# Performance work log

Measured on AMD Instinct MI355X. Metric: run time of the kernel, lower is better.

## Reference

```python
import jax, jax.numpy as jnp
import numpy as np

N = 100000      # nodes
E = 1600000     # edges (avg degree 16)
D = 128         # feature dim (in_dim == out_dim)
ALPHA = 0.1     # initial-residual mixing
BETA = 0.5      # identity-mapping / linear mixing


def setup_inputs() -> dict:
    key = jax.random.key(0)
    k1, k2, k3, k4, k5 = jax.random.split(key, 5)
    features = jax.random.normal(k1, (N, D), dtype=jnp.float32)
    initial_features = jax.random.normal(k2, (N, D), dtype=jnp.float32)
    # xavier_uniform with relu gain sqrt(2): bound = gain * sqrt(6/(fan_in+fan_out))
    bound = np.sqrt(2.0) * np.sqrt(6.0 / (D + D))
    W = jax.random.uniform(k5, (D, D), dtype=jnp.float32, minval=-bound, maxval=bound)
    src = jax.random.randint(k3, (E,), 0, N, dtype=jnp.int32)
    dst = jax.random.randint(k4, (E,), 0, N, dtype=jnp.int32)
    return {"features": features, "initial_features": initial_features,
            "W": W, "src": src, "dst": dst}


def reference(features, initial_features, W, src, dst):
    # symmetric degree normalization (edge weights are all ones)
    degs = jax.ops.segment_sum(jnp.ones((E,), features.dtype), dst, num_segments=N)
    norm = jnp.power(jnp.maximum(degs, 1.0), -0.5)[:, None]          # [N,1]
    h = features * norm                                               # [N,D]
    # message passing: m_e = h[src_e] * w_e (w=1); aggregate sum into dst
    agg = jax.ops.segment_sum(h[src], dst, num_segments=N)            # [N,D]
    h = agg * norm
    # alpha initial-residual, beta identity-mapped linear combine
    h = (1.0 - ALPHA) * h + ALPHA * initial_features
    h = (1.0 - BETA) * h + BETA * (h @ W.T)
    return jax.nn.relu(h)
```

## Files before the change

### kernel.cpp

```cpp
#include <hip/hip_runtime.h>
#include <math.h>

#define D 128
#define THREADS 256
#define BS 512
#define MAXB 1024
#define BIN_T 512
#define BIN_CHUNK 4096

typedef __attribute__((ext_vector_type(8))) short s16x8;
typedef __attribute__((ext_vector_type(4))) float f32x4;

__device__ __forceinline__ unsigned short f2bf(float f) {
    unsigned u = __float_as_uint(f);
    u += 0x7FFFu + ((u >> 16) & 1u);
    return (unsigned short)(u >> 16);
}
__device__ __forceinline__ float bflo(unsigned u) { return __uint_as_float(u << 16); }
__device__ __forceinline__ float bfhi(unsigned u) { return __uint_as_float(u & 0xFFFF0000u); }


__global__ __launch_bounds__(THREADS) void k_hist(const int* __restrict__ dst,
                                                  int* __restrict__ bcnt,
                                                  int E, int nbuck) {
    __shared__ int lh[MAXB];
    for (int b = threadIdx.x; b < nbuck; b += THREADS) lh[b] = 0;
    __syncthreads();
    const int stride = gridDim.x * THREADS;
    for (int e = blockIdx.x * THREADS + threadIdx.x; e < E; e += stride)
        atomicAdd(&lh[dst[e] >> 9], 1);
    __syncthreads();
    for (int b = threadIdx.x; b < nbuck; b += THREADS) {
        const int v = lh[b];
        if (v) atomicAdd(&bcnt[b], v);
    }
}

__global__ __launch_bounds__(MAXB) void k_scan(const int* __restrict__ bcnt,
                                               int* __restrict__ bbase,
                                               int* __restrict__ bcur, int nbuck) {
    __shared__ int sh[MAXB];
    const int tid = threadIdx.x;
    const int v = (tid < nbuck) ? bcnt[tid] : 0;
    sh[tid] = v;
    __syncthreads();
    for (int s = 1; s < MAXB; s <<= 1) {
        const int t = (tid >= s) ? sh[tid - s] : 0;
        __syncthreads();
        sh[tid] += t;
        __syncthreads();
    }
    if (tid < nbuck) {
        const int ex = sh[tid] - v;
        bbase[tid] = ex;
        bcur[tid] = ex;
    }
    if (tid == nbuck - 1) bbase[nbuck] = sh[tid];
}

__global__ __launch_bounds__(BIN_T) void k_bin(const int* __restrict__ src,
                                               const int* __restrict__ dst,
                                               int* __restrict__ bcur,
                                               int2* __restrict__ ebuf,
                                               int E, int nbuck) {
    __shared__ int lh[MAXB];
    __shared__ int lbase[MAXB];
    const int tid = threadIdx.x;
    for (int b = tid; b < nbuck; b += BIN_T) lh[b] = 0;
    __syncthreads();
    const int base = blockIdx.x * BIN_CHUNK;
    int2 ed[8];
#pragma unroll
    for (int k = 0; k < 8; ++k) {
        const int e = base + k * BIN_T + tid;
        if (e < E) {
            ed[k] = make_int2(dst[e], src[e]);
            atomicAdd(&lh[ed[k].x >> 9], 1);
        } else {
            ed[k].x = -1;
        }
    }
    __syncthreads();
    for (int b = tid; b < nbuck; b += BIN_T) {
        const int v = lh[b];
        lbase[b] = v ? atomicAdd(&bcur[b], v) : 0;
        lh[b] = 0;
    }
    __syncthreads();
#pragma unroll
    for (int k = 0; k < 8; ++k) {
        if (ed[k].x >= 0) {
            const int b = ed[k].x >> 9;
            const int pos = lbase[b] + atomicAdd(&lh[b], 1);
            ebuf[pos] = ed[k];
        }
    }
}

__global__ __launch_bounds__(BS) void k_csr(const int* __restrict__ bbase,
                                            const int2* __restrict__ ebuf,
                                            int* __restrict__ csr,
                                            int* __restrict__ off,
                                            float* __restrict__ normf,
                                            int n, int nbuck) {
    __shared__ int cnt[BS];
    __shared__ int ex[BS];
    const int b = blockIdx.x, tid = threadIdx.x;
    const int lo = bbase[b], hi = bbase[b + 1];
    cnt[tid] = 0;
    __syncthreads();
    for (int e = lo + tid; e < hi; e += BS)
        atomicAdd(&cnt[ebuf[e].x & (BS - 1)], 1);
    __syncthreads();
    const int deg = cnt[tid];
    ex[tid] = deg;
    __syncthreads();
    for (int s = 1; s < BS; s <<= 1) {
        const int t = (tid >= s) ? ex[tid - s] : 0;
        __syncthreads();
        ex[tid] += t;
        __syncthreads();
    }
    const int excl = ex[tid] - deg;
    const int node = b * BS + tid;
    if (node < n) {
        off[node] = lo + excl;
        normf[node] = rsqrtf(fmaxf((float)deg, 1.0f));
    }
    if (b == nbuck - 1 && tid == 0) off[n] = bbase[nbuck];
    cnt[tid] = excl;
    __syncthreads();
    for (int e = lo + tid; e < hi; e += BS) {
        const int2 edge = ebuf[e];
        const int p = atomicAdd(&cnt[edge.x & (BS - 1)], 1);
        csr[lo + p] = edge.y;
    }
}

__global__ __launch_bounds__(THREADS) void k_scale(
    const float* __restrict__ f, const float* __restrict__ nrm,
    uint4* __restrict__ hb, int n) {
    int c = blockIdx.x * THREADS + threadIdx.x;
    if (c >= n * 16) return;
    float nv = nrm[c >> 4];
    const float4* fp = (const float4*)f;
    float4 a = fp[c * 2], b = fp[c * 2 + 1];
    uint4 o;
    o.x = f2bf(a.x * nv) | ((unsigned)f2bf(a.y * nv) << 16);
    o.y = f2bf(a.z * nv) | ((unsigned)f2bf(a.w * nv) << 16);
    o.z = f2bf(b.x * nv) | ((unsigned)f2bf(b.y * nv) << 16);
    o.w = f2bf(b.z * nv) | ((unsigned)f2bf(b.w * nv) << 16);
    hb[c] = o;
}

__global__ __launch_bounds__(THREADS) void k_gather_csr(
    const uint4* __restrict__ hb, const float* __restrict__ initf,
    const int* __restrict__ off, const int* __restrict__ csr,
    const float* __restrict__ normf, uint4* __restrict__ tb, int n) {
    const int g = (blockIdx.x * THREADS + threadIdx.x) >> 4;
    if (g >= n) return;
    const int gl = threadIdx.x & 15;

    float acc[8] = {0.f, 0.f, 0.f, 0.f, 0.f, 0.f, 0.f, 0.f};

#define ROW(S)                                                      \
    {                                                               \
        const uint4 r = hb[(size_t)(S)*16 + gl];                    \
        acc[0] += bflo(r.x); acc[1] += bfhi(r.x);                   \
        acc[2] += bflo(r.y); acc[3] += bfhi(r.y);                   \
        acc[4] += bflo(r.z); acc[5] += bfhi(r.z);                   \
        acc[6] += bflo(r.w); acc[7] += bfhi(r.w);                   \
    }
    const int begin = off[g], end = off[g + 1];
    int j = begin;
    for (; j + 4 <= end; j += 4) {
        const int s0 = csr[j], s1 = csr[j + 1], s2 = csr[j + 2], s3 = csr[j + 3];
        ROW(s0); ROW(s1); ROW(s2); ROW(s3);
    }
    for (; j < end; ++j) ROW(csr[j]);
#undef ROW

    const float nv = 0.9f * normf[g];
    const float4* iv = (const float4*)(initf + (size_t)g * D);
    const float4 i0 = iv[gl * 2], i1 = iv[gl * 2 + 1];
    float t[8];
    t[0] = nv * acc[0] + 0.1f * i0.x; t[1] = nv * acc[1] + 0.1f * i0.y;
    t[2] = nv * acc[2] + 0.1f * i0.z; t[3] = nv * acc[3] + 0.1f * i0.w;
    t[4] = nv * acc[4] + 0.1f * i1.x; t[5] = nv * acc[5] + 0.1f * i1.y;
    t[6] = nv * acc[6] + 0.1f * i1.z; t[7] = nv * acc[7] + 0.1f * i1.w;
    uint4 o;
    o.x = f2bf(t[0]) | ((unsigned)f2bf(t[1]) << 16);
    o.y = f2bf(t[2]) | ((unsigned)f2bf(t[3]) << 16);
    o.z = f2bf(t[4]) | ((unsigned)f2bf(t[5]) << 16);
    o.w = f2bf(t[6]) | ((unsigned)f2bf(t[7]) << 16);
    tb[(size_t)g * 16 + gl] = o;
}

__device__ __forceinline__ void stage_M(const float* __restrict__ W,
                                        uint4* __restrict__ sMt, int tid) {
    for (int c = tid; c < D * 16; c += THREADS) {
        const int j = c >> 4, kc = c & 15;
        const float* wr = W + j * D + kc * 8;
        float m[8];
#pragma unroll
        for (int q = 0; q < 8; ++q) m[q] = 0.5f * wr[q];
        const int dj = j - kc * 8;
        if (dj >= 0 && dj < 8) m[dj] += 0.5f;
        uint4 o;
        o.x = f2bf(m[0]) | ((unsigned)f2bf(m[1]) << 16);
        o.y = f2bf(m[2]) | ((unsigned)f2bf(m[3]) << 16);
        o.z = f2bf(m[4]) | ((unsigned)f2bf(m[5]) << 16);
        o.w = f2bf(m[6]) | ((unsigned)f2bf(m[7]) << 16);
        sMt[j * 16 + (kc ^ (j & 7))] = o;
    }
}

__device__ __forceinline__ void gemm_tile(const uint4* __restrict__ sMt,
                                          const uint4* __restrict__ sT,
                                          float* __restrict__ out,
                                          int base, int n, int lane, int wave) {
    const int l15 = lane & 15, lq = lane >> 4;
    const int mt = wave & 1, ntb = (wave >> 1) * 4;
    const int nr = mt * 16 + l15;
    s16x8 a[4];
#pragma unroll
    for (int ks = 0; ks < 4; ++ks)
        a[ks] = *reinterpret_cast<const s16x8*>(
            &sT[nr * 16 + ((ks * 4 + lq) ^ (nr & 7))]);

#pragma unroll
    for (int tnt = 0; tnt < 4; ++tnt) {
        const int nt = ntb + tnt;
        const int jr = nt * 16 + l15;
        f32x4 c = {0.f, 0.f, 0.f, 0.f};
#pragma unroll
        for (int ks = 0; ks < 4; ++ks) {
            const s16x8 b = *reinterpret_cast<const s16x8*>(
                &sMt[jr * 16 + ((ks * 4 + lq) ^ (jr & 7))]);
            c = __builtin_amdgcn_mfma_f32_16x16x32_bf16(a[ks], b, c, 0, 0, 0);
        }
        const int col = nt * 16 + l15;
        const int row0 = base + mt * 16 + lq * 4;
#pragma unroll
        for (int r = 0; r < 4; ++r) {
            const int node = row0 + r;
            if (node < n) out[(size_t)node * D + col] = fmaxf(c[r], 0.f);
        }
    }
}

__global__ __launch_bounds__(THREADS) void k_gemm_tb(
    const float* __restrict__ W, const uint4* __restrict__ tb,
    float* __restrict__ out, int n, int numTiles) {
    __shared__ uint4 sMt[D * 16];
    __shared__ uint4 sT[32 * 16];
    const int tid = threadIdx.x;
    stage_M(W, sMt, tid);
    __syncthreads();

    const int sn = tid >> 3;
    const int c0 = (tid & 7) * 2;
    const int wave = tid >> 6, lane = tid & 63;

    for (int tile = blockIdx.x; tile < numTiles; tile += gridDim.x) {
        const int base = tile << 5;
        {
            const int node = base + sn;
#pragma unroll
            for (int s = 0; s < 2; ++s) {
                const int cc = c0 + s;
                uint4 o;
                if (node < n) o = tb[(size_t)node * 16 + cc];
                else o.x = o.y = o.z = o.w = 0u;
                sT[sn * 16 + (cc ^ (sn & 7))] = o;
            }
        }
        __syncthreads();
        gemm_tile(sMt, sT, out, base, n, lane, wave);
        __syncthreads();
    }
}

__global__ __launch_bounds__(THREADS) void k_build1(
    const int* __restrict__ src, const int* __restrict__ dst,
    int* __restrict__ head, int2* __restrict__ p, int E) {
    int e = blockIdx.x * THREADS + threadIdx.x;
    if (e < E) {
        int nx = atomicExch(&head[dst[e]], e);
        p[e] = make_int2(nx, src[e]);
    }
}

__global__ __launch_bounds__(THREADS) void k_normwalk1(
    const int* __restrict__ head, const int2* __restrict__ p,
    float* __restrict__ normf, int n) {
    int i = blockIdx.x * THREADS + threadIdx.x;
    if (i >= n) return;
    int c = head[i], cnt = 0;
    while (c >= 0) { ++cnt; c = p[c].x; }
    normf[i] = rsqrtf(fmaxf((float)cnt, 1.0f));
}

__global__ __launch_bounds__(THREADS) void k_gatherchain(
    const float* __restrict__ features, const float* __restrict__ initf,
    const int* __restrict__ head, const int2* __restrict__ p,
    const float* __restrict__ normf, float* __restrict__ out, int n) {
    const int g = (blockIdx.x * THREADS + threadIdx.x) >> 4;
    if (g >= n) return;
    const int gl = threadIdx.x & 15;
    float acc[8] = {0.f, 0.f, 0.f, 0.f, 0.f, 0.f, 0.f, 0.f};
    int c = head[g];
    while (c >= 0) {
        const int2 pc = p[c];
        const float w = normf[pc.y];
        const float4* fr = (const float4*)(features + (size_t)pc.y * D);
        const float4 f0 = fr[gl * 2], f1 = fr[gl * 2 + 1];
        acc[0] += f0.x * w; acc[1] += f0.y * w;
        acc[2] += f0.z * w; acc[3] += f0.w * w;
        acc[4] += f1.x * w; acc[5] += f1.y * w;
        acc[6] += f1.z * w; acc[7] += f1.w * w;
        c = pc.x;
    }
    const float nv = 0.9f * normf[g];
    const float4* iv = (const float4*)(initf + (size_t)g * D);
    const float4 i0 = iv[gl * 2], i1 = iv[gl * 2 + 1];
    float4 t0, t1;
    t0.x = nv * acc[0] + 0.1f * i0.x; t0.y = nv * acc[1] + 0.1f * i0.y;
    t0.z = nv * acc[2] + 0.1f * i0.z; t0.w = nv * acc[3] + 0.1f * i0.w;
    t1.x = nv * acc[4] + 0.1f * i1.x; t1.y = nv * acc[5] + 0.1f * i1.y;
    t1.z = nv * acc[6] + 0.1f * i1.z; t1.w = nv * acc[7] + 0.1f * i1.w;
    float4* orow = (float4*)(out + (size_t)g * D);
    orow[gl * 2] = t0;
    orow[gl * 2 + 1] = t1;
}

__global__ __launch_bounds__(THREADS) void k_gemm_ip(
    const float* __restrict__ W, float* __restrict__ out, int n, int numTiles) {
    __shared__ uint4 sMt[D * 16];
    __shared__ uint4 sT[32 * 16];
    const int tid = threadIdx.x;
    stage_M(W, sMt, tid);
    __syncthreads();
    const int sn = tid >> 3;
    const int c0 = (tid & 7) * 2;
    const int wave = tid >> 6, lane = tid & 63;
    for (int tile = blockIdx.x; tile < numTiles; tile += gridDim.x) {
        const int base = tile << 5;
        {
            const int node = base + sn;
#pragma unroll
            for (int s = 0; s < 2; ++s) {
                const int cc = c0 + s;
                uint4 o;
                if (node < n) {
                    const float4* tr = (const float4*)(out + (size_t)node * D);
                    const float4 a = tr[cc * 2], b = tr[cc * 2 + 1];
                    o.x = f2bf(a.x) | ((unsigned)f2bf(a.y) << 16);
                    o.y = f2bf(a.z) | ((unsigned)f2bf(a.w) << 16);
                    o.z = f2bf(b.x) | ((unsigned)f2bf(b.y) << 16);
                    o.w = f2bf(b.z) | ((unsigned)f2bf(b.w) << 16);
                } else {
                    o.x = o.y = o.z = o.w = 0u;
                }
                sT[sn * 16 + (cc ^ (sn & 7))] = o;
            }
        }
        __syncthreads();
        gemm_tile(sMt, sT, out, base, n, lane, wave);
        __syncthreads();
    }
}

extern "C" void kernel_launch(void* const* d_in, const int* in_sizes, int n_in,
                              void* d_out, int out_size, void* d_ws, size_t ws_size,
                              hipStream_t stream) {
    const float* features = (const float*)d_in[0];
    const float* initf    = (const float*)d_in[1];
    const float* W        = (const float*)d_in[2];
    const int*   src      = (const int*)d_in[3];
    const int*   dst      = (const int*)d_in[4];
    float* out = (float*)d_out;

    const int n = in_sizes[0] / D;
    const int E = in_sizes[3];
    if (n <= 0) return;

    const int nbuck = (n + BS - 1) / BS;
    const int numTiles = (n + 31) >> 5;
    const int gridT = numTiles < 1024 ? numTiles : 1024;
    const int gridG = (int)(((size_t)n * 16 + THREADS - 1) / THREADS);

    const size_t nA   = ((size_t)n * 4 + 15) & ~(size_t)15;
    const size_t oA   = ((size_t)(n + 1) * 4 + 15) & ~(size_t)15;
    const size_t bA   = ((size_t)(MAXB + 1) * 4 + 15) & ~(size_t)15;
    const size_t eA   = ((size_t)E * 8 + 15) & ~(size_t)15;
    const size_t cA   = ((size_t)E * 4 + 15) & ~(size_t)15;
    const size_t hbA  = (size_t)n * 256;
    const size_t tbA  = (size_t)n * 256;
    const size_t needMain = nA + oA + 3 * bA + eA + cA + hbA + tbA;

    if (nbuck <= MAXB && ws_size >= needMain) {
        char* w = (char*)d_ws;
        float* normf = (float*)w;                 w += nA;
        int*   off   = (int*)w;                   w += oA;
        int*   bcnt  = (int*)w;                   w += bA;
        int*   bbase = (int*)w;                   w += bA;
        int*   bcur  = (int*)w;                   w += bA;
        int2*  ebuf  = (int2*)w;                  w += eA;
        int*   csr   = (int*)w;                   w += cA;
        uint4* hb    = (uint4*)w;                 w += hbA;
        uint4* tb    = (uint4*)w;

        hipMemsetAsync(bcnt, 0, (size_t)(MAXB + 1) * 4, stream);
        k_hist<<<256, THREADS, 0, stream>>>(dst, bcnt, E, nbuck);
        k_scan<<<1, MAXB, 0, stream>>>(bcnt, bbase, bcur, nbuck);
        k_bin<<<(E + BIN_CHUNK - 1) / BIN_CHUNK, BIN_T, 0, stream>>>(
            src, dst, bcur, ebuf, E, nbuck);
        k_csr<<<nbuck, BS, 0, stream>>>(bbase, ebuf, csr, off, normf, n, nbuck);
        k_scale<<<(n * 16 + THREADS - 1) / THREADS, THREADS, 0, stream>>>(
            features, normf, hb, n);
        k_gather_csr<<<gridG, THREADS, 0, stream>>>(hb, initf, off, csr, normf, tb, n);
        k_gemm_tb<<<gridT, THREADS, 0, stream>>>(W, tb, out, n, numTiles);
    } else {
        const size_t pA = ((size_t)E * 8 + 15) & ~(size_t)15;
        float* normf = (float*)d_ws;
        int*   head  = (int*)((char*)d_ws + nA);
        int2*  p     = (int2*)((char*)d_ws + 2 * nA);
        if (ws_size < 2 * nA + pA) return;
        hipMemsetAsync(head, 0xFF, (size_t)n * 4, stream);
        k_build1<<<(E + THREADS - 1) / THREADS, THREADS, 0, stream>>>(src, dst, head, p, E);
        k_normwalk1<<<(n + THREADS - 1) / THREADS, THREADS, 0, stream>>>(head, p, normf, n);
        k_gatherchain<<<gridG, THREADS, 0, stream>>>(features, initf, head, p, normf, out, n);
        k_gemm_ip<<<gridT, THREADS, 0, stream>>>(W, out, n, numTiles);
    }
}
```

Baseline: 179.9 us.

## Phase gather by source range, add nontemporal loads/stores, larger bin chunks

The CSR gather now walks each node's neighbor list four times, each pass accumulating only sources in one quarter of the node range. The aim is to keep the gathered bf16 rows of each pass resident in cache, and neighbor indices are now read as int4 vectors. Streaming loads and stores (features, initial features, the tb intermediate, output) become nontemporal so they do not evict the gather working set. Binning also handles 16 edges per thread instead of 8. The trade-off is four passes over the index lists with divergent branches. The int4 load of csr + j also assumes 16-byte alignment that begin does not guarantee.

After: 231.2 us. +28.5%, slower.

```diff
diff --git a/kernel.cpp b/kernel.cpp
--- a/kernel.cpp
+++ b/kernel.cpp
@@ -6,10 +6,13 @@
 #define BS 512
 #define MAXB 1024
 #define BIN_T 512
-#define BIN_CHUNK 4096
+#define EPT 16
+#define BIN_CHUNK (BIN_T * EPT)
 
 typedef __attribute__((ext_vector_type(8))) short s16x8;
 typedef __attribute__((ext_vector_type(4))) float f32x4;
+typedef __attribute__((ext_vector_type(4))) float f4;
+typedef __attribute__((ext_vector_type(4))) unsigned u4;
 
 __device__ __forceinline__ unsigned short f2bf(float f) {
     unsigned u = __float_as_uint(f);
@@ -69,9 +72,9 @@
     for (int b = tid; b < nbuck; b += BIN_T) lh[b] = 0;
     __syncthreads();
     const int base = blockIdx.x * BIN_CHUNK;
-    int2 ed[8];
-#pragma unroll
-    for (int k = 0; k < 8; ++k) {
+    int2 ed[EPT];
+#pragma unroll
+    for (int k = 0; k < EPT; ++k) {
         const int e = base + k * BIN_T + tid;
         if (e < E) {
             ed[k] = make_int2(dst[e], src[e]);
@@ -88,7 +91,7 @@
     }
     __syncthreads();
 #pragma unroll
-    for (int k = 0; k < 8; ++k) {
+    for (int k = 0; k < EPT; ++k) {
         if (ed[k].x >= 0) {
             const int b = ed[k].x >> 9;
             const int pos = lbase[b] + atomicAdd(&lh[b], 1);
@@ -143,8 +146,9 @@
     int c = blockIdx.x * THREADS + threadIdx.x;
     if (c >= n * 16) return;
     float nv = nrm[c >> 4];
-    const float4* fp = (const float4*)f;
-    float4 a = fp[c * 2], b = fp[c * 2 + 1];
+    const f4* fp = (const f4*)f;
+    const f4 a = __builtin_nontemporal_load(fp + c * 2);
+    const f4 b = __builtin_nontemporal_load(fp + c * 2 + 1);
     uint4 o;
     o.x = f2bf(a.x * nv) | ((unsigned)f2bf(a.y * nv) << 16);
     o.y = f2bf(a.z * nv) | ((unsigned)f2bf(a.w * nv) << 16);
@@ -172,28 +176,40 @@
         acc[6] += bflo(r.w); acc[7] += bfhi(r.w);                   \
     }
     const int begin = off[g], end = off[g + 1];
-    int j = begin;
-    for (; j + 4 <= end; j += 4) {
-        const int s0 = csr[j], s1 = csr[j + 1], s2 = csr[j + 2], s3 = csr[j + 3];
-        ROW(s0); ROW(s1); ROW(s2); ROW(s3);
-    }
-    for (; j < end; ++j) ROW(csr[j]);
+    const unsigned cut = ((unsigned)n + 3) >> 2;
+#pragma unroll 1
+    for (int ph = 0; ph < 4; ++ph) {
+        const unsigned plo = ph * cut;
+        int j = begin;
+        for (; j + 4 <= end; j += 4) {
+            const int4 s4 = *reinterpret_cast<const int4*>(csr + j);
+            if ((unsigned)(s4.x - plo) < cut) ROW(s4.x);
+            if ((unsigned)(s4.y - plo) < cut) ROW(s4.y);
+            if ((unsigned)(s4.z - plo) < cut) ROW(s4.z);
+            if ((unsigned)(s4.w - plo) < cut) ROW(s4.w);
+        }
+        for (; j < end; ++j) {
+            const int s = csr[j];
+            if ((unsigned)(s - plo) < cut) ROW(s);
+        }
+    }
 #undef ROW
 
     const float nv = 0.9f * normf[g];
-    const float4* iv = (const float4*)(initf + (size_t)g * D);
-    const float4 i0 = iv[gl * 2], i1 = iv[gl * 2 + 1];
+    const f4* iv = (const f4*)(initf + (size_t)g * D);
+    const f4 i0 = __builtin_nontemporal_load(iv + gl * 2);
+    const f4 i1 = __builtin_nontemporal_load(iv + gl * 2 + 1);
     float t[8];
     t[0] = nv * acc[0] + 0.1f * i0.x; t[1] = nv * acc[1] + 0.1f * i0.y;
     t[2] = nv * acc[2] + 0.1f * i0.z; t[3] = nv * acc[3] + 0.1f * i0.w;
     t[4] = nv * acc[4] + 0.1f * i1.x; t[5] = nv * acc[5] + 0.1f * i1.y;
     t[6] = nv * acc[6] + 0.1f * i1.z; t[7] = nv * acc[7] + 0.1f * i1.w;
-    uint4 o;
+    u4 o;
     o.x = f2bf(t[0]) | ((unsigned)f2bf(t[1]) << 16);
     o.y = f2bf(t[2]) | ((unsigned)f2bf(t[3]) << 16);
     o.z = f2bf(t[4]) | ((unsigned)f2bf(t[5]) << 16);
     o.w = f2bf(t[6]) | ((unsigned)f2bf(t[7]) << 16);
-    tb[(size_t)g * 16 + gl] = o;
+    __builtin_nontemporal_store(o, (u4*)tb + (size_t)g * 16 + gl);
 }
 
 __device__ __forceinline__ void stage_M(const float* __restrict__ W,
@@ -244,7 +260,9 @@
 #pragma unroll
         for (int r = 0; r < 4; ++r) {
             const int node = row0 + r;
-            if (node < n) out[(size_t)node * D + col] = fmaxf(c[r], 0.f);
+            if (node < n)
+                __builtin_nontemporal_store(fmaxf(c[r], 0.f),
+                                            &out[(size_t)node * D + col]);
         }
     }
 }
@@ -270,8 +288,13 @@
             for (int s = 0; s < 2; ++s) {
                 const int cc = c0 + s;
                 uint4 o;
-                if (node < n) o = tb[(size_t)node * 16 + cc];
-                else o.x = o.y = o.z = o.w = 0u;
+                if (node < n) {
+                    const u4 t = __builtin_nontemporal_load(
+                        (const u4*)tb + (size_t)node * 16 + cc);
+                    o.x = t.x; o.y = t.y; o.z = t.z; o.w = t.w;
+                } else {
+                    o.x = o.y = o.z = o.w = 0u;
+                }
                 sT[sn * 16 + (cc ^ (sn & 7))] = o;
             }
         }
```
